# Performance work log

Hardware: AMD Instinct MI355X
Metric: run time of the kernel (lower is better)

The kernel has to match this reference:

```python
import jax, jax.numpy as jnp
import numpy as np

N_NODES = 100000
N_EDGES = 3200000
N_GRAPHS = 256
IN_CH = 8
HID = 64
N_REL = 2


def rgcn_conv(x, edge_index, edge_type, W, root, bias):
    # W: [R, in, out]; PyG RGCNConv with aggr='mean' per relation, summed across relations
    n = x.shape[0]
    src, dst = edge_index[0], edge_index[1]
    H = jnp.einsum('ni,rio->rno', x, W)                      # [R, N, out]
    msgs = H[edge_type, src]                                  # [E, out]
    # per-(node, relation) in-degree for the mean
    seg = dst * N_REL + edge_type
    deg = jax.ops.segment_sum(jnp.ones_like(edge_type, dtype=x.dtype), seg,
                              num_segments=n * N_REL)
    norm = jnp.maximum(deg[seg], 1.0)
    agg = jax.ops.segment_sum(msgs / norm[:, None], dst, num_segments=n)  # [N, out]
    return agg + x @ root + bias


def setup_inputs() -> dict:
    key = jax.random.key(0)
    ks = jax.random.split(key, 16)
    x = jax.random.normal(ks[0], (N_NODES, IN_CH), dtype=jnp.float32)
    edge_index = jax.random.randint(ks[1], (2, N_EDGES), 0, N_NODES, dtype=jnp.int64)
    edge_type = jax.random.randint(ks[2], (N_EDGES,), 0, N_REL, dtype=jnp.int64)
    batch = jnp.sort(jax.random.randint(ks[3], (N_NODES,), 0, N_GRAPHS, dtype=jnp.int64))

    def glorot(k, shape):
        fan_in, fan_out = shape[-2], shape[-1]
        s = float(np.sqrt(6.0 / (fan_in + fan_out)))
        return jax.random.uniform(k, shape, dtype=jnp.float32, minval=-s, maxval=s)

    params = {
        'W1': glorot(ks[4], (N_REL, IN_CH, HID)), 'root1': glorot(ks[5], (IN_CH, HID)),
        'b1': jnp.zeros((HID,), jnp.float32),
        'W2': glorot(ks[6], (N_REL, HID, HID)), 'root2': glorot(ks[7], (HID, HID)),
        'b2': jnp.zeros((HID,), jnp.float32),
        'W3': glorot(ks[8], (N_REL, HID, HID)), 'root3': glorot(ks[9], (HID, HID)),
        'b3': jnp.zeros((HID,), jnp.float32),
        'cW1': glorot(ks[10], (HID, HID // 2)), 'cb1': jnp.zeros((HID // 2,), jnp.float32),
        'cW2': glorot(ks[11], (HID // 2, 1)), 'cb2': jnp.zeros((1,), jnp.float32),
    }
    return {'x': x, 'edge_index': edge_index, 'edge_type': edge_type, 'batch': batch, **params}


def reference(x, edge_index, edge_type, batch,
              W1, root1, b1, W2, root2, b2, W3, root3, b3,
              cW1, cb1, cW2, cb2):
    h = jax.nn.relu(rgcn_conv(x, edge_index, edge_type, W1, root1, b1))
    h = jax.nn.relu(rgcn_conv(h, edge_index, edge_type, W2, root2, b2))
    h = rgcn_conv(h, edge_index, edge_type, W3, root3, b3)
    g = jax.ops.segment_sum(h, batch, num_segments=N_GRAPHS)   # global_add_pool
    # dropout is identity in eval mode
    g = jax.nn.relu(g @ cW1 + cb1)
    return g @ cW2 + cb2                                        # [N_GRAPHS, 1]
```

## Files before the change

### kernel.cpp

```cpp
#include <hip/hip_runtime.h>


typedef unsigned int uint;
typedef unsigned short ushort;
typedef __attribute__((ext_vector_type(8))) short bf16x8;
typedef __attribute__((ext_vector_type(4))) float f32x4;

#define EPB 12288
#define BCAP 8960

__device__ __forceinline__ void fma4(float4& a, float s, const float4& w){
  a.x += s*w.x; a.y += s*w.y; a.z += s*w.z; a.w += s*w.w;
}
__device__ __forceinline__ uint bf1(float f){
  uint u = __float_as_uint(f);
  return (u + 0x7fffu + ((u>>16)&1u)) >> 16;
}
__device__ __forceinline__ uint bfpack2(float lo, float hi){
  return bf1(lo) | (bf1(hi)<<16);
}
__device__ __forceinline__ float4 bf4cvt(uint2 w){
  float4 r;
  r.x = __uint_as_float(w.x<<16);
  r.y = __uint_as_float(w.x & 0xffff0000u);
  r.z = __uint_as_float(w.y<<16);
  r.w = __uint_as_float(w.y & 0xffff0000u);
  return r;
}
__device__ __forceinline__ void addf4(float4& a, const float4& f){
  a.x += f.x; a.y += f.y; a.z += f.z; a.w += f.w;
}
__device__ __forceinline__ void fmacf4(float4& a, float s, const float4& f){
  a.x = fmaf(s, f.x, a.x); a.y = fmaf(s, f.y, a.y);
  a.z = fmaf(s, f.z, a.z); a.w = fmaf(s, f.w, a.w);
}
__device__ __forceinline__ void redf4(float4& a){
  a.x += __shfl_xor(a.x,16); a.x += __shfl_xor(a.x,32);
  a.y += __shfl_xor(a.y,16); a.y += __shfl_xor(a.y,32);
  a.z += __shfl_xor(a.z,16); a.z += __shfl_xor(a.z,32);
  a.w += __shfl_xor(a.w,16); a.w += __shfl_xor(a.w,32);
}

__global__ __launch_bounds__(256) void k_prep(
    const float* __restrict__ W2, const float* __restrict__ root2,
    const float* __restrict__ W3, const float* __restrict__ root3,
    ushort* __restrict__ wt2, ushort* __restrict__ wt3,
    int* __restrict__ bcur, float* __restrict__ gp, int NBK, int G){
  int b = blockIdx.x, t = threadIdx.x;
  if (b < 2){
    const float* Wl = b ? W3 : W2;
    const float* rp = b ? root3 : root2;
    ushort* wt = b ? wt3 : wt2;
    for (int i = t; i < 64*192; i += 256){
      int n = i / 192, k = i - n*192;
      float v = (k < 128) ? Wl[k*64 + n] : rp[(k-128)*64 + n];
      wt[i] = (ushort)bf1(v);
    }
  } else {
    for (int i = t; i < NBK; i += 256) bcur[i] = i * BCAP;
    for (int i = t; i < G*64; i += 256) gp[i] = 0.f;
  }
}

__global__ __launch_bounds__(1024) void k_part(const int* __restrict__ ei,
    const int* __restrict__ et, int* __restrict__ bcur,
    uint* __restrict__ bk, int E, int NBK){
  __shared__ int h[400];
  __shared__ int cur[400];
  int t = threadIdx.x;
  for (int i=t;i<NBK;i+=1024) h[i]=0;
  __syncthreads();
  int base = blockIdx.x*EPB;
  for (int i=t; i<EPB; i+=1024){
    int e = base+i;
    if (e < E) atomicAdd(&h[ei[E+e]>>8], 1);
  }
  __syncthreads();
  for (int i=t;i<NBK;i+=1024){
    int c = h[i];
    cur[i] = c ? atomicAdd(&bcur[i], c) : 0;
  }
  __syncthreads();
  for (int i=t; i<EPB; i+=4096){
    int e0=base+i, e1=base+i+1024, e2=base+i+2048, e3=base+i+3072;
    bool v0=e0<E, v1=e1<E, v2=e2<E, v3=e3<E;
    int s0=0,d0=0,y0=0,s1=0,d1=0,y1=0,s2=0,d2=0,y2=0,s3=0,d3=0,y3=0;
    if (v0){ s0=ei[e0]; d0=ei[E+e0]; y0=et[e0]; }
    if (v1){ s1=ei[e1]; d1=ei[E+e1]; y1=et[e1]; }
    if (v2){ s2=ei[e2]; d2=ei[E+e2]; y2=et[e2]; }
    if (v3){ s3=ei[e3]; d3=ei[E+e3]; y3=et[e3]; }
    if (v0){
      int bu=d0>>8, p=atomicAdd(&cur[bu],1);
      if (p < (bu+1)*BCAP) bk[p] = ((uint)s0<<9)|(uint)(((d0&255)<<1)|y0);
    }
    if (v1){
      int bu=d1>>8, p=atomicAdd(&cur[bu],1);
      if (p < (bu+1)*BCAP) bk[p] = ((uint)s1<<9)|(uint)(((d1&255)<<1)|y1);
    }
    if (v2){
      int bu=d2>>8, p=atomicAdd(&cur[bu],1);
      if (p < (bu+1)*BCAP) bk[p] = ((uint)s2<<9)|(uint)(((d2&255)<<1)|y2);
    }
    if (v3){
      int bu=d3>>8, p=atomicAdd(&cur[bu],1);
      if (p < (bu+1)*BCAP) bk[p] = ((uint)s3<<9)|(uint)(((d3&255)<<1)|y3);
    }
  }
}

__global__ __launch_bounds__(1024) void k_csr(const uint* __restrict__ bk,
    const int* __restrict__ bcur, int* __restrict__ deg,
    int* __restrict__ pos, int* __restrict__ ssrc, int N){
  __shared__ int h[512];
  __shared__ int cur[512];
  __shared__ int ws[256];
  int b = blockIdx.x, t = threadIdx.x;
  int start = b*BCAP;
  int end = bcur[b];
  int lim = (b+1)*BCAP; if (end > lim) end = lim;
  if (t < 512) h[t]=0;
  __syncthreads();
  for (int i=start+t; i<end; i+=1024) atomicAdd(&h[bk[i]&511], 1);
  __syncthreads();
  int c0=0, c1=0, s=0;
  if (t < 256){
    c0=h[2*t]; c1=h[2*t+1]; s=c0+c1;
    ws[t] = s;
  }
  __syncthreads();
  for (int off=1; off<256; off<<=1){
    int tmp = (t>=off && t<256)? ws[t-off]:0;
    __syncthreads();
    if (t<256) ws[t] += tmp;
    __syncthreads();
  }
  if (t < 256){
    int base0 = start + ws[t] - s;
    cur[2*t]   = base0;
    cur[2*t+1] = base0 + c0;
    int node = (b<<8) + t;
    if (node < N){
      deg[(b<<9)+2*t]   = c0; deg[(b<<9)+2*t+1] = c1;
      pos[(b<<9)+2*t]   = base0; pos[(b<<9)+2*t+1] = base0 + c0;
    }
  }
  __syncthreads();
  for (int i=start+t; i<end; i+=1024){
    uint w = bk[i];
    int p = atomicAdd(&cur[w & 511], 1);
    ssrc[p] = (int)(w >> 9);
  }
}

__global__ __launch_bounds__(256) void k_gather64(
    const ushort* __restrict__ hp, const int* __restrict__ deg,
    const int* __restrict__ pos, const int* __restrict__ ssrc,
    ushort* __restrict__ sn, int N)
{
  int lane = threadIdx.x & 63;
  int wid  = (blockIdx.x*256 + threadIdx.x) >> 6;
  int c4 = lane & 15, eg = lane >> 4;
  int nA = wid*2, nB = nA+1;
  if (nA >= N) return;
  int d0A = deg[2*nA], d1A = deg[2*nA+1];
  int pA  = pos[2*nA];
  int cA  = d0A + d1A;
  int d0B = 0, d1B = 0, pB = 0, cB = 0;
  if (nB < N){ d0B = deg[2*nB]; d1B = deg[2*nB+1]; pB = pos[2*nB]; cB = d0B+d1B; }

  float4 totA={0,0,0,0}, difA={0,0,0,0}, totB={0,0,0,0}, difB={0,0,0,0};
  int jA = 0, jB = 0;
  while (jA < cA || jB < cB){
    int tA = cA - jA; if (tA > 64) tA = 64;
    int tB = cB - jB; if (tB > 64) tB = 64;
    int svA = (lane < tA) ? ssrc[pA + jA + lane] : 0;
    int svB = (lane < tB) ? ssrc[pB + jB + lane] : 0;
    int mt = tA > tB ? tA : tB;
    for (int e = 0; e < mt; e += 4){
      int idx = e + eg;
      int siA = __shfl(svA, idx), siB = __shfl(svB, idx);
      uint2 wA = {0u,0u}, wB = {0u,0u};
      if (idx < tA) wA = *(const uint2*)(hp + (size_t)siA*64 + c4*4);
      if (idx < tB) wB = *(const uint2*)(hp + (size_t)siB*64 + c4*4);
      float4 fA = bf4cvt(wA), fB = bf4cvt(wB);
      float sgA = ((jA + idx) < d0A) ? 1.f : -1.f;
      float sgB = ((jB + idx) < d0B) ? 1.f : -1.f;
      addf4(totA, fA); fmacf4(difA, sgA, fA);
      addf4(totB, fB); fmacf4(difB, sgB, fB);
    }
    jA += tA; jB += tB;
  }
  redf4(totA); redf4(difA); redf4(totB); redf4(difB);
  int rel = (lane >> 4) & 1;
  float4 tt_ = (lane < 32) ? totA : totB;
  float4 dd_ = (lane < 32) ? difA : difB;
  int dsel = (lane < 32) ? (rel ? d1A : d0A) : (rel ? d1B : d0B);
  float sg = rel ? -1.f : 1.f;
  float id = 0.5f / (float)(dsel > 1 ? dsel : 1);
  float4 v;
  v.x = fmaf(sg, dd_.x, tt_.x) * id;
  v.y = fmaf(sg, dd_.y, tt_.y) * id;
  v.z = fmaf(sg, dd_.z, tt_.z) * id;
  v.w = fmaf(sg, dd_.w, tt_.w) * id;
  int n = (lane < 32) ? nA : nB;
  if (n < N){
    uint2 pkt; pkt.x = bfpack2(v.x, v.y); pkt.y = bfpack2(v.z, v.w);
    *(uint2*)(sn + (size_t)n*128 + rel*64 + c4*4) = pkt;
  }
}

__global__ __launch_bounds__(256) void k_gather8(
    const float* __restrict__ xp, const int* __restrict__ deg,
    const int* __restrict__ pos, const int* __restrict__ ssrc,
    float* __restrict__ sn1, int N)
{
  int lane = threadIdx.x & 63;
  int wid  = (blockIdx.x*256 + threadIdx.x) >> 6;
  int c = lane & 7, eg = lane >> 3;
  int nA = wid*2, nB = nA+1;
  if (nA >= N) return;
  int d0A = deg[2*nA], d1A = deg[2*nA+1];
  int pA  = pos[2*nA];
  int cA  = d0A + d1A;
  int d0B = 0, d1B = 0, pB = 0, cB = 0;
  if (nB < N){ d0B = deg[2*nB]; d1B = deg[2*nB+1]; pB = pos[2*nB]; cB = d0B+d1B; }

  float totA=0.f, s1A=0.f, totB=0.f, s1B=0.f;
  int jA = 0, jB = 0;
  while (jA < cA || jB < cB){
    int tA = cA - jA; if (tA > 64) tA = 64;
    int tB = cB - jB; if (tB > 64) tB = 64;
    int svA = (lane < tA) ? ssrc[pA + jA + lane] : 0;
    int svB = (lane < tB) ? ssrc[pB + jB + lane] : 0;
    int mt = tA > tB ? tA : tB;
    for (int e = 0; e < mt; e += 8){
      int idx = e + eg;
      int siA = __shfl(svA, idx), siB = __shfl(svB, idx);
      float vA = 0.f, vB = 0.f;
      if (idx < tA) vA = xp[(size_t)siA*8 + c];
      if (idx < tB) vB = xp[(size_t)siB*8 + c];
      totA += vA;  s1A += ((jA + idx) >= d0A) ? vA : 0.f;
      totB += vB;  s1B += ((jB + idx) >= d0B) ? vB : 0.f;
    }
    jA += tA; jB += tB;
  }
  float s0A = totA - s1A, s0B = totB - s1B;
  #pragma unroll
  for (int off=8; off<64; off<<=1){
    s0A += __shfl_xor(s0A, off); s1A += __shfl_xor(s1A, off);
    s0B += __shfl_xor(s0B, off); s1B += __shfl_xor(s1B, off);
  }
  s0A *= 1.f/(float)(d0A>1?d0A:1);  s1A *= 1.f/(float)(d1A>1?d1A:1);
  s0B *= 1.f/(float)(d0B>1?d0B:1);  s1B *= 1.f/(float)(d1B>1?d1B:1);
  if (lane < 32){
    float v = (lane < 16) ? ((lane & 8) ? s1A : s0A)
                          : ((lane & 8) ? s1B : s0B);
    int n = (lane < 16) ? nA : nB;
    if (n < N) sn1[(size_t)n*16 + (lane & 15)] = v;
  }
}

template<int RELU, int OUTBF>
__global__ __launch_bounds__(256) void k_mm192m(
    const ushort* __restrict__ sn,
    const ushort* __restrict__ hp,
    const ushort* __restrict__ wt,
    const float* __restrict__ bias, void* __restrict__ hout_, int N)
{
  int t = threadIdx.x, lane = t & 63, w = t >> 6;
  int quad = lane >> 4, l15 = lane & 15;
  int nb = blockIdx.x * 64;
  int node = nb + w*16 + l15;
  int ncl = node < N ? node : N-1;
  const ushort* arow_sn = sn + (size_t)ncl*128 + quad*8;
  const ushort* arow_hp = hp + (size_t)ncl*64  + quad*8;

  f32x4 acc0={0,0,0,0}, acc1={0,0,0,0}, acc2={0,0,0,0}, acc3={0,0,0,0};
  #pragma unroll
  for (int ks = 0; ks < 6; ++ks){
    bf16x8 a = (ks < 4) ? *(const bf16x8*)(arow_sn + ks*32)
                        : *(const bf16x8*)(arow_hp + (ks-4)*32);
    const ushort* wk = wt + (size_t)l15*192 + ks*32 + quad*8;
    bf16x8 b0 = *(const bf16x8*)(wk);
    bf16x8 b1 = *(const bf16x8*)(wk + 16*192);
    bf16x8 b2 = *(const bf16x8*)(wk + 32*192);
    bf16x8 b3 = *(const bf16x8*)(wk + 48*192);
    acc0 = __builtin_amdgcn_mfma_f32_16x16x32_bf16(a, b0, acc0, 0,0,0);
    acc1 = __builtin_amdgcn_mfma_f32_16x16x32_bf16(a, b1, acc1, 0,0,0);
    acc2 = __builtin_amdgcn_mfma_f32_16x16x32_bf16(a, b2, acc2, 0,0,0);
    acc3 = __builtin_amdgcn_mfma_f32_16x16x32_bf16(a, b3, acc3, 0,0,0);
  }
  f32x4 accs[4] = {acc0, acc1, acc2, acc3};
  #pragma unroll
  for (int tt = 0; tt < 4; ++tt){
    int n = tt*16 + l15;
    float bv = bias[n];
    #pragma unroll
    for (int i = 0; i < 4; ++i){
      int nd = nb + w*16 + quad*4 + i;
      if (nd < N){
        float v = accs[tt][i] + bv;
        if (RELU) v = fmaxf(v, 0.f);
        if (OUTBF) ((ushort*)hout_)[(size_t)nd*64 + n] = (ushort)bf1(v);
        else       ((float*)hout_)[(size_t)nd*64 + n] = v;
      }
    }
  }
}

__global__ __launch_bounds__(256) void k_mm192pool(
    const ushort* __restrict__ sn, const ushort* __restrict__ hp,
    const ushort* __restrict__ wt, const float* __restrict__ bias,
    const int* __restrict__ batch, float* __restrict__ gp, int N)
{
  __shared__ float hl[64*66];
  __shared__ int bl[64];
  int t = threadIdx.x, lane = t & 63, w = t >> 6;
  int quad = lane >> 4, l15 = lane & 15;
  int nb = blockIdx.x * 64;
  int node = nb + w*16 + l15;
  int ncl = node < N ? node : N-1;
  const ushort* arow_sn = sn + (size_t)ncl*128 + quad*8;
  const ushort* arow_hp = hp + (size_t)ncl*64  + quad*8;

  f32x4 acc0={0,0,0,0}, acc1={0,0,0,0}, acc2={0,0,0,0}, acc3={0,0,0,0};
  #pragma unroll
  for (int ks = 0; ks < 6; ++ks){
    bf16x8 a = (ks < 4) ? *(const bf16x8*)(arow_sn + ks*32)
                        : *(const bf16x8*)(arow_hp + (ks-4)*32);
    const ushort* wk = wt + (size_t)l15*192 + ks*32 + quad*8;
    bf16x8 b0 = *(const bf16x8*)(wk);
    bf16x8 b1 = *(const bf16x8*)(wk + 16*192);
    bf16x8 b2 = *(const bf16x8*)(wk + 32*192);
    bf16x8 b3 = *(const bf16x8*)(wk + 48*192);
    acc0 = __builtin_amdgcn_mfma_f32_16x16x32_bf16(a, b0, acc0, 0,0,0);
    acc1 = __builtin_amdgcn_mfma_f32_16x16x32_bf16(a, b1, acc1, 0,0,0);
    acc2 = __builtin_amdgcn_mfma_f32_16x16x32_bf16(a, b2, acc2, 0,0,0);
    acc3 = __builtin_amdgcn_mfma_f32_16x16x32_bf16(a, b3, acc3, 0,0,0);
  }
  f32x4 accs[4] = {acc0, acc1, acc2, acc3};
  #pragma unroll
  for (int tt = 0; tt < 4; ++tt){
    int ch = tt*16 + l15;
    float bv = bias[ch];
    #pragma unroll
    for (int i = 0; i < 4; ++i){
      int nl = w*16 + quad*4 + i;
      hl[nl*66 + ch] = accs[tt][i] + bv;
    }
  }
  if (t < 64) bl[t] = (nb + t < N) ? batch[nb + t] : -1;
  __syncthreads();
  int c = t & 63, q = t >> 6;
  float acc = 0.f; int curg = -1;
  #pragma unroll 4
  for (int i = 0; i < 16; ++i){
    int nl = q*16 + i;
    int g = bl[nl];
    if (g != curg){
      if (curg >= 0) atomicAdd(&gp[curg*64 + c], acc);
      curg = g; acc = 0.f;
    }
    if (g >= 0) acc += hl[nl*66 + c];
  }
  if (curg >= 0) atomicAdd(&gp[curg*64 + c], acc);
}

__global__ __launch_bounds__(256) void k_mm24(
    const float* __restrict__ sn1,
    const float* __restrict__ xp,
    const float* __restrict__ Wl,
    const float* __restrict__ rootp,
    const float* __restrict__ bias, ushort* __restrict__ hout, int N)
{
  __shared__ float A[64*25];
  int t = threadIdx.x;
  int nb = blockIdx.x*64;
  #pragma unroll
  for (int k=0;k<4;++k){
    int q = k*256 + t;
    int nl = q>>4, c = q&15;
    int n = nb + nl;
    A[nl*25 + c] = (n < N) ? sn1[(size_t)n*16 + c] : 0.f;
  }
  #pragma unroll
  for (int k=0;k<2;++k){
    int q = k*256 + t;
    int nl = q>>3, c = q&7;
    int n = nb + nl;
    A[nl*25 + 16 + c] = (n < N) ? xp[(size_t)n*8 + c] : 0.f;
  }
  __syncthreads();
  int o0=(t&15)*4, r0=(t>>4)*4;
  float4 b4 = *(const float4*)(bias+o0);
  float4 a0=b4,a1=b4,a2=b4,a3=b4;
  const float* Ab=&A[r0*25];
  #pragma unroll
  for (int i=0;i<16;++i){
    float4 w=*(const float4*)(Wl+i*64+o0);
    fma4(a0,Ab[i],w); fma4(a1,Ab[25+i],w); fma4(a2,Ab[50+i],w); fma4(a3,Ab[75+i],w);
  }
  #pragma unroll
  for (int i=0;i<8;++i){
    float4 w=*(const float4*)(rootp+i*64+o0);
    fma4(a0,Ab[16+i],w); fma4(a1,Ab[41+i],w); fma4(a2,Ab[66+i],w); fma4(a3,Ab[91+i],w);
  }
  float4 accs[4]={a0,a1,a2,a3};
  #pragma unroll
  for (int q=0;q<4;++q){
    int n = nb + r0 + q;
    if (n < N){
      float4 r = accs[q];
      r.x=fmaxf(r.x,0.f); r.y=fmaxf(r.y,0.f); r.z=fmaxf(r.z,0.f); r.w=fmaxf(r.w,0.f);
      uint2 p; p.x = bfpack2(r.x,r.y); p.y = bfpack2(r.z,r.w);
      *(uint2*)(hout + (size_t)n*64 + o0) = p;
    }
  }
}

__global__ __launch_bounds__(256) void k_clf(const float* __restrict__ gp,
    const float* __restrict__ cW1, const float* __restrict__ cb1,
    const float* __restrict__ cW2, const float* __restrict__ cb2,
    float* __restrict__ out, int G){
  int lane = threadIdx.x & 63;
  int g = (blockIdx.x*256 + threadIdx.x) >> 6;
  if (g >= G) return;
  int j = lane & 31, half = lane >> 5;
  const float* gv = gp + (size_t)g*64 + half*32;
  const float* Wc = cW1 + half*32*32 + j;
  float s = 0.f;
  #pragma unroll 8
  for (int i=0;i<32;++i) s += gv[i] * Wc[i*32];
  s += __shfl_xor(s, 32);
  s = fmaxf(s + cb1[j], 0.f) * cW2[j];
  s += __shfl_xor(s, 1);  s += __shfl_xor(s, 2);
  s += __shfl_xor(s, 4);  s += __shfl_xor(s, 8);
  s += __shfl_xor(s, 16);
  if (lane == 0) out[g] = s + cb2[0];
}

extern "C" void kernel_launch(void* const* d_in, const int* in_sizes, int n_in,
                              void* d_out, int out_size, void* d_ws, size_t ws_size,
                              hipStream_t stream){
  const float* x     = (const float*)d_in[0];
  const int*   ei    = (const int*)d_in[1];
  const int*   et    = (const int*)d_in[2];
  const int*   batch = (const int*)d_in[3];
  const float* W1    = (const float*)d_in[4];
  const float* root1 = (const float*)d_in[5];
  const float* b1    = (const float*)d_in[6];
  const float* W2    = (const float*)d_in[7];
  const float* root2 = (const float*)d_in[8];
  const float* b2    = (const float*)d_in[9];
  const float* W3    = (const float*)d_in[10];
  const float* root3 = (const float*)d_in[11];
  const float* b3    = (const float*)d_in[12];
  const float* cW1   = (const float*)d_in[13];
  const float* cb1   = (const float*)d_in[14];
  const float* cW2   = (const float*)d_in[15];
  const float* cb2   = (const float*)d_in[16];
  float* out = (float*)d_out;
  (void)n_in; (void)ws_size;

  int N = in_sizes[0]/8;
  int E = in_sizes[2];
  int G = out_size;
  int M = 2*N;
  int NBK = (N + 255) >> 8;

  char* w = (char*)d_ws;
  auto alloc=[&](size_t bytes)->char*{ char* p=w; w += (bytes+255)&~(size_t)255; return p; };
  int*    bcur  = (int*)alloc(1024*4);
  int*    ssrc  = (int*)alloc((size_t)NBK*BCAP*4);
  int*    deg   = (int*)alloc((size_t)M*4);
  int*    pos   = (int*)alloc((size_t)M*4);
  ushort* h1    = (ushort*)alloc((size_t)N*64*2);
  ushort* snU   = (ushort*)alloc((size_t)N*128*2);
  ushort* h2    = (ushort*)alloc((size_t)N*64*2);
  float*  gp    = (float*)alloc((size_t)G*64*4);
  ushort* wt2   = (ushort*)alloc(64*192*2);
  ushort* wt3   = (ushort*)alloc(64*192*2);
  uint*   bk    = (uint*)snU;
  float*  sn1   = (float*)snU;

  k_prep<<<3,256,0,stream>>>(W2,root2,W3,root3,wt2,wt3,bcur,gp,NBK,G);
  int nbE = (E + EPB - 1)/EPB;
  k_part <<<nbE,1024,0,stream>>>(ei,et,bcur,bk,E,NBK);
  k_csr  <<<NBK,1024,0,stream>>>(bk,bcur,deg,pos,ssrc,N);

  int gb = (((N+1)/2) + 3) / 4;
  int nbk = (N+63)/64;
  k_gather8 <<<gb,256,0,stream>>>(x,deg,pos,ssrc,sn1,N);
  k_mm24    <<<nbk,256,0,stream>>>(sn1,x,W1,root1,b1,h1,N);
  k_gather64<<<gb,256,0,stream>>>(h1,deg,pos,ssrc,snU,N);
  k_mm192m<1,1><<<nbk,256,0,stream>>>(snU,h1,wt2,b2,h2,N);
  k_gather64<<<gb,256,0,stream>>>(h2,deg,pos,ssrc,snU,N);
  k_mm192pool<<<nbk,256,0,stream>>>(snU,h2,wt3,b3,batch,gp,N);
  k_clf<<<(G*64+255)/256,256,0,stream>>>(gp,cW1,cb1,cW2,cb2,out,G);
}
```

Measured before the change: 384.9 us.

## Fold prep kernel into CSR build, memset bucket counters, unroll partition and gather

Removes the separate k_prep launch. The weight transpose/bf16 conversion and the pool-buffer zeroing move into two extra blocks of k_csr, and bucket cursors are zeroed with a memset and now hold relative counts. The partition kernel halves edges per block and processes its six edges per thread in one straight-line pass instead of a loop. The gather loop is unrolled to issue eight row loads per iteration instead of four, to get more memory-level parallelism. The trade-off is more partition blocks hitting the global atomics and higher register pressure in the gather.

```diff
diff --git a/kernel.cpp b/kernel.cpp
--- a/kernel.cpp
+++ b/kernel.cpp
@@ -6,7 +6,7 @@
 typedef __attribute__((ext_vector_type(8))) short bf16x8;
 typedef __attribute__((ext_vector_type(4))) float f32x4;
 
-#define EPB 12288
+#define EPB 6144
 #define BCAP 8960
 
 __device__ __forceinline__ void fma4(float4& a, float s, const float4& w){
@@ -41,27 +41,6 @@
   a.w += __shfl_xor(a.w,16); a.w += __shfl_xor(a.w,32);
 }
 
-__global__ __launch_bounds__(256) void k_prep(
-    const float* __restrict__ W2, const float* __restrict__ root2,
-    const float* __restrict__ W3, const float* __restrict__ root3,
-    ushort* __restrict__ wt2, ushort* __restrict__ wt3,
-    int* __restrict__ bcur, float* __restrict__ gp, int NBK, int G){
-  int b = blockIdx.x, t = threadIdx.x;
-  if (b < 2){
-    const float* Wl = b ? W3 : W2;
-    const float* rp = b ? root3 : root2;
-    ushort* wt = b ? wt3 : wt2;
-    for (int i = t; i < 64*192; i += 256){
-      int n = i / 192, k = i - n*192;
-      float v = (k < 128) ? Wl[k*64 + n] : rp[(k-128)*64 + n];
-      wt[i] = (ushort)bf1(v);
-    }
-  } else {
-    for (int i = t; i < NBK; i += 256) bcur[i] = i * BCAP;
-    for (int i = t; i < G*64; i += 256) gp[i] = 0.f;
-  }
-}
-
 __global__ __launch_bounds__(1024) void k_part(const int* __restrict__ ei,
     const int* __restrict__ et, int* __restrict__ bcur,
     uint* __restrict__ bk, int E, int NBK){
@@ -78,46 +57,74 @@
   __syncthreads();
   for (int i=t;i<NBK;i+=1024){
     int c = h[i];
-    cur[i] = c ? atomicAdd(&bcur[i], c) : 0;
-  }
-  __syncthreads();
-  for (int i=t; i<EPB; i+=4096){
-    int e0=base+i, e1=base+i+1024, e2=base+i+2048, e3=base+i+3072;
-    bool v0=e0<E, v1=e1<E, v2=e2<E, v3=e3<E;
-    int s0=0,d0=0,y0=0,s1=0,d1=0,y1=0,s2=0,d2=0,y2=0,s3=0,d3=0,y3=0;
-    if (v0){ s0=ei[e0]; d0=ei[E+e0]; y0=et[e0]; }
-    if (v1){ s1=ei[e1]; d1=ei[E+e1]; y1=et[e1]; }
-    if (v2){ s2=ei[e2]; d2=ei[E+e2]; y2=et[e2]; }
-    if (v3){ s3=ei[e3]; d3=ei[E+e3]; y3=et[e3]; }
-    if (v0){
-      int bu=d0>>8, p=atomicAdd(&cur[bu],1);
-      if (p < (bu+1)*BCAP) bk[p] = ((uint)s0<<9)|(uint)(((d0&255)<<1)|y0);
-    }
-    if (v1){
-      int bu=d1>>8, p=atomicAdd(&cur[bu],1);
-      if (p < (bu+1)*BCAP) bk[p] = ((uint)s1<<9)|(uint)(((d1&255)<<1)|y1);
-    }
-    if (v2){
-      int bu=d2>>8, p=atomicAdd(&cur[bu],1);
-      if (p < (bu+1)*BCAP) bk[p] = ((uint)s2<<9)|(uint)(((d2&255)<<1)|y2);
-    }
-    if (v3){
-      int bu=d3>>8, p=atomicAdd(&cur[bu],1);
-      if (p < (bu+1)*BCAP) bk[p] = ((uint)s3<<9)|(uint)(((d3&255)<<1)|y3);
-    }
+    cur[i] = c ? (i*BCAP + atomicAdd(&bcur[i], c)) : 0;
+  }
+  __syncthreads();
+  int e0=base+t,      e1=base+t+1024, e2=base+t+2048;
+  int e3=base+t+3072, e4=base+t+4096, e5=base+t+5120;
+  bool v0=e0<E, v1=e1<E, v2=e2<E, v3=e3<E, v4=e4<E, v5=e5<E;
+  int s0=0,d0=0,y0=0,s1=0,d1=0,y1=0,s2=0,d2=0,y2=0;
+  int s3=0,d3=0,y3=0,s4=0,d4=0,y4=0,s5=0,d5=0,y5=0;
+  if (v0){ s0=ei[e0]; d0=ei[E+e0]; y0=et[e0]; }
+  if (v1){ s1=ei[e1]; d1=ei[E+e1]; y1=et[e1]; }
+  if (v2){ s2=ei[e2]; d2=ei[E+e2]; y2=et[e2]; }
+  if (v3){ s3=ei[e3]; d3=ei[E+e3]; y3=et[e3]; }
+  if (v4){ s4=ei[e4]; d4=ei[E+e4]; y4=et[e4]; }
+  if (v5){ s5=ei[e5]; d5=ei[E+e5]; y5=et[e5]; }
+  if (v0){
+    int bu=d0>>8, p=atomicAdd(&cur[bu],1);
+    if (p < (bu+1)*BCAP) bk[p] = ((uint)s0<<9)|(uint)(((d0&255)<<1)|y0);
+  }
+  if (v1){
+    int bu=d1>>8, p=atomicAdd(&cur[bu],1);
+    if (p < (bu+1)*BCAP) bk[p] = ((uint)s1<<9)|(uint)(((d1&255)<<1)|y1);
+  }
+  if (v2){
+    int bu=d2>>8, p=atomicAdd(&cur[bu],1);
+    if (p < (bu+1)*BCAP) bk[p] = ((uint)s2<<9)|(uint)(((d2&255)<<1)|y2);
+  }
+  if (v3){
+    int bu=d3>>8, p=atomicAdd(&cur[bu],1);
+    if (p < (bu+1)*BCAP) bk[p] = ((uint)s3<<9)|(uint)(((d3&255)<<1)|y3);
+  }
+  if (v4){
+    int bu=d4>>8, p=atomicAdd(&cur[bu],1);
+    if (p < (bu+1)*BCAP) bk[p] = ((uint)s4<<9)|(uint)(((d4&255)<<1)|y4);
+  }
+  if (v5){
+    int bu=d5>>8, p=atomicAdd(&cur[bu],1);
+    if (p < (bu+1)*BCAP) bk[p] = ((uint)s5<<9)|(uint)(((d5&255)<<1)|y5);
   }
 }
 
 __global__ __launch_bounds__(1024) void k_csr(const uint* __restrict__ bk,
     const int* __restrict__ bcur, int* __restrict__ deg,
-    int* __restrict__ pos, int* __restrict__ ssrc, int N){
+    int* __restrict__ pos, int* __restrict__ ssrc, int N,
+    const float* __restrict__ W2, const float* __restrict__ root2,
+    const float* __restrict__ W3, const float* __restrict__ root3,
+    ushort* __restrict__ wt2, ushort* __restrict__ wt3,
+    float* __restrict__ gp, int NBK, int G){
+  int b = blockIdx.x, t = threadIdx.x;
+  if (b >= NBK){
+    const float* Wl = (b==NBK) ? W2 : W3;
+    const float* rp = (b==NBK) ? root2 : root3;
+    ushort* wt = (b==NBK) ? wt2 : wt3;
+    for (int i=t; i<64*192; i+=1024){
+      int n = i/192, k = i - n*192;
+      float v = (k<128) ? Wl[k*64+n] : rp[(k-128)*64+n];
+      wt[i] = (ushort)bf1(v);
+    }
+    if (b==NBK+1){
+      for (int i=t;i<G*64;i+=1024) gp[i]=0.f;
+    }
+    return;
+  }
   __shared__ int h[512];
   __shared__ int cur[512];
   __shared__ int ws[256];
-  int b = blockIdx.x, t = threadIdx.x;
   int start = b*BCAP;
-  int end = bcur[b];
-  int lim = (b+1)*BCAP; if (end > lim) end = lim;
+  int cnt = bcur[b]; if (cnt > BCAP) cnt = BCAP;
+  int end = start + cnt;
   if (t < 512) h[t]=0;
   __syncthreads();
   for (int i=start+t; i<end; i+=1024) atomicAdd(&h[bk[i]&511], 1);
@@ -176,17 +183,25 @@
     int svA = (lane < tA) ? ssrc[pA + jA + lane] : 0;
     int svB = (lane < tB) ? ssrc[pB + jB + lane] : 0;
     int mt = tA > tB ? tA : tB;
-    for (int e = 0; e < mt; e += 4){
-      int idx = e + eg;
-      int siA = __shfl(svA, idx), siB = __shfl(svB, idx);
-      uint2 wA = {0u,0u}, wB = {0u,0u};
-      if (idx < tA) wA = *(const uint2*)(hp + (size_t)siA*64 + c4*4);
-      if (idx < tB) wB = *(const uint2*)(hp + (size_t)siB*64 + c4*4);
-      float4 fA = bf4cvt(wA), fB = bf4cvt(wB);
-      float sgA = ((jA + idx) < d0A) ? 1.f : -1.f;
-      float sgB = ((jB + idx) < d0B) ? 1.f : -1.f;
-      addf4(totA, fA); fmacf4(difA, sgA, fA);
-      addf4(totB, fB); fmacf4(difB, sgB, fB);
+    for (int e = 0; e < mt; e += 8){
+      int i0 = e + eg, i1 = e + 4 + eg;
+      int siA0 = __shfl(svA, i0), siB0 = __shfl(svB, i0);
+      int siA1 = __shfl(svA, i1), siB1 = __shfl(svB, i1);
+      uint2 wA0={0u,0u}, wB0={0u,0u}, wA1={0u,0u}, wB1={0u,0u};
+      if (i0 < tA) wA0 = *(const uint2*)(hp + (size_t)siA0*64 + c4*4);
+      if (i0 < tB) wB0 = *(const uint2*)(hp + (size_t)siB0*64 + c4*4);
+      if (i1 < tA) wA1 = *(const uint2*)(hp + (size_t)siA1*64 + c4*4);
+      if (i1 < tB) wB1 = *(const uint2*)(hp + (size_t)siB1*64 + c4*4);
+      float4 fA0 = bf4cvt(wA0), fB0 = bf4cvt(wB0);
+      float4 fA1 = bf4cvt(wA1), fB1 = bf4cvt(wB1);
+      float sgA0 = ((jA + i0) < d0A) ? 1.f : -1.f;
+      float sgB0 = ((jB + i0) < d0B) ? 1.f : -1.f;
+      float sgA1 = ((jA + i1) < d0A) ? 1.f : -1.f;
+      float sgB1 = ((jB + i1) < d0B) ? 1.f : -1.f;
+      addf4(totA, fA0); fmacf4(difA, sgA0, fA0);
+      addf4(totB, fB0); fmacf4(difB, sgB0, fB0);
+      addf4(totA, fA1); fmacf4(difA, sgA1, fA1);
+      addf4(totB, fB1); fmacf4(difB, sgB1, fB1);
     }
     jA += tA; jB += tB;
   }
@@ -483,10 +498,11 @@
   uint*   bk    = (uint*)snU;
   float*  sn1   = (float*)snU;
 
-  k_prep<<<3,256,0,stream>>>(W2,root2,W3,root3,wt2,wt3,bcur,gp,NBK,G);
+  hipMemsetAsync(bcur, 0, (size_t)NBK*4, stream);
   int nbE = (E + EPB - 1)/EPB;
   k_part <<<nbE,1024,0,stream>>>(ei,et,bcur,bk,E,NBK);
-  k_csr  <<<NBK,1024,0,stream>>>(bk,bcur,deg,pos,ssrc,N);
+  k_csr  <<<NBK+2,1024,0,stream>>>(bk,bcur,deg,pos,ssrc,N,
+                                   W2,root2,W3,root3,wt2,wt3,gp,NBK,G);
 
   int gb = (((N+1)/2) + 3) / 4;
   int nbk = (N+63)/64;
```

Result: faster. 368.3 us (-4.3%).
